# Kernel optimization log

Hardware: AMD Instinct MI355X
Metric: run time of the kernel (lower is better)

The kernel has to match this reference:

```python
import jax, jax.numpy as jnp
import numpy as np

S = 4096          # sequence length (must equal d_model due to the module's v-transpose bug)
D = 4096          # d_model; n_head = heads = 1, bs = 1
SCALE = 64.0      # scale_factor = sqrt(d_model)
W_STD = 0.02      # weight init scale to keep softmax logits sane


def setup_inputs() -> dict:
    k0 = jax.random.key(0)
    ks = jax.random.split(k0, 8)
    return {
        "query": jax.random.normal(ks[0], (1, S, D), jnp.float32),
        "key":   jax.random.normal(ks[1], (1, S, D), jnp.float32),
        "value": jax.random.normal(ks[2], (1, S, D), jnp.float32),
        "Wq": jax.random.normal(ks[3], (D, D), jnp.float32) * W_STD,
        "bq": jnp.zeros((D,), jnp.float32),
        "Wk": jax.random.normal(ks[4], (D, D), jnp.float32) * W_STD,
        "bk": jnp.zeros((D,), jnp.float32),
        "Wv": jax.random.normal(ks[5], (D, D), jnp.float32) * W_STD,
        "bv": jnp.zeros((D,), jnp.float32),
        "Wo": jax.random.normal(ks[6], (D, D), jnp.float32) * W_STD,
        "bo": jnp.zeros((D,), jnp.float32),
    }


def reference(query, key, value, Wq, bq, Wk, bk, Wv, bv, Wo, bo):
    # Linear projections (torch Linear: x @ W.T + b). n_head = 1, so out dim = D.
    q = query @ Wq.T + bq                       # [1, S, D]
    k = key   @ Wk.T + bk                       # [1, S, D]
    v = value @ Wv.T + bv                       # [1, S, D]
    # k.reshape(bs, heads, -1, d_model).transpose(2, 3) -> [1, 1, D, S]
    k4 = k.reshape(1, 1, S, D).transpose(0, 1, 3, 2)
    # v gets the SAME (buggy) transpose -> [1, 1, D, S]
    v4 = v.reshape(1, 1, S, D).transpose(0, 1, 3, 2)
    # q [1,S,D] broadcasts against k4 [1,1,D,S] -> scores [1,1,S,S]
    scores = jnp.matmul(q[:, None], k4) / SCALE
    attn = jax.nn.softmax(scores, axis=-1)      # [1, 1, S, S]
    # dropout_p = 0 / eval mode -> identity
    ctx = jnp.matmul(attn, v4)                  # [1, 1, S, D] (S == D)
    out = ctx @ Wo.T + bo + value[:, None]      # residual add, broadcast to [1,1,S,D]
    return out.reshape(1, -1, D)                # [1, S, D]
```

## Files before the change

kernel.cpp:

```cpp
#include <hip/hip_runtime.h>


typedef __attribute__((ext_vector_type(4))) float f32x4;
typedef __attribute__((ext_vector_type(8))) short short8;
typedef __attribute__((ext_vector_type(4))) unsigned short us4;

#define DIM 4096
#define NT  64

__device__ __forceinline__ unsigned short f2bf(float f) {
    unsigned int u = __builtin_bit_cast(unsigned int, f);
    u += 0x7fffu + ((u >> 16) & 1u);
    return (unsigned short)(u >> 16);
}

__device__ __forceinline__ void gll16(const void* g, void* l) {
    __builtin_amdgcn_global_load_lds(
        (const __attribute__((address_space(1))) unsigned int*)g,
        (__attribute__((address_space(3))) unsigned int*)l,
        16, 0, 0);
}

__global__ void cast_kernel(const float* __restrict__ in, unsigned short* __restrict__ out) {
    const size_t i = ((size_t)blockIdx.x * 256 + threadIdx.x) * 4;
    float4 x = *(const float4*)(in + i);
    us4 y;
    y.x = f2bf(x.x); y.y = f2bf(x.y); y.z = f2bf(x.z); y.w = f2bf(x.w);
    *(us4*)(out + i) = y;
}

template <int EPI>
__global__ __launch_bounds__(512, 2)
void gemm256(const unsigned short* __restrict__ A, const unsigned short* __restrict__ B,
             void* __restrict__ Cout, const float* __restrict__ bias,
             const float* __restrict__ res) {
    __shared__ alignas(16) char lds[131072];

    const int tid = threadIdx.x;
    const int w = tid >> 6, l = tid & 63;
    const int wr = w >> 2, wc = w & 3;

    const int bid = blockIdx.x;
    const int swz = (bid & 7) * 32 + (bid >> 3);
    const int row0 = (swz >> 4) << 8;
    const int col0 = (swz & 15) << 8;

    const int laneA  = (l & 15) * 64 + ((((l >> 4) << 4)) ^ ((l & 8) << 2));
    const int sl_row = l >> 2;
    const int sl_col = ((l & 3) << 3) ^ ((l & 32) ? 16 : 0);

    f32x4 acc[8][4];
    const f32x4 zero = {0.f, 0.f, 0.f, 0.f};
#pragma unroll
    for (int m = 0; m < 8; ++m)
#pragma unroll
        for (int n = 0; n < 4; ++n) acc[m][n] = zero;

    char* const ldsp = (char*)lds;

    auto stage = [&](const unsigned short* __restrict__ M, char* ldsMat, int rowbase,
                     int t, int h) {
        {
            const int rg = h * 8 + (w >> 1), cg = w & 1;
            gll16(M + (size_t)(rowbase + rg * 16 + sl_row) * DIM + t * 64 + cg * 32 + sl_col,
                  ldsMat + ((rg * 2 + cg) << 10));
        }
        {
            const int s = 8 + w;
            const int rg = h * 8 + (s >> 1), cg = s & 1;
            gll16(M + (size_t)(rowbase + rg * 16 + sl_row) * DIM + t * 64 + cg * 32 + sl_col,
                  ldsMat + ((rg * 2 + cg) << 10));
        }
    };

    stage(A, ldsp,          row0, 0, 0);
    stage(A, ldsp,          row0, 0, 1);
    stage(B, ldsp + 32768,  col0, 0, 0);
    stage(B, ldsp + 32768,  col0, 0, 1);
    stage(A, ldsp + 65536,  row0, 1, 0);
    asm volatile("s_waitcnt vmcnt(2)\ns_barrier" ::: "memory");

#pragma unroll 1
    for (int t = 0; t < NT; ++t) {
        const char* Ab = ldsp + (t & 1) * 65536;
        const char* Bb = Ab + 32768;
        const int t1 = (t + 1 < NT) ? t + 1 : NT - 1;
        const int t2 = (t + 2 < NT) ? t + 2 : NT - 1;
        char* A1 = ldsp + (t1 & 1) * 65536;
        char* B1 = A1 + 32768;
        char* A2 = ldsp + (t2 & 1) * 65536;

        const int aoff = wr * 16384 + laneA;
        const int boff = wc * 8192 + laneA;

        short8 a[4][2], b0[2][2], b1[2][2];

#pragma unroll
        for (int m2 = 0; m2 < 4; ++m2)
#pragma unroll
            for (int ks = 0; ks < 2; ++ks)
                a[m2][ks] = *(const short8*)(Ab + aoff + ((m2 * 2 + ks) << 10));
#pragma unroll
        for (int n2 = 0; n2 < 2; ++n2)
#pragma unroll
            for (int ks = 0; ks < 2; ++ks)
                b0[n2][ks] = *(const short8*)(Bb + boff + ((n2 * 2 + ks) << 10));
        stage(A, A1, row0, t1, 1);
        __builtin_amdgcn_s_barrier();
        asm volatile("s_waitcnt lgkmcnt(0)");
        __builtin_amdgcn_s_setprio(1);
#pragma unroll
        for (int m2 = 0; m2 < 4; ++m2)
#pragma unroll
            for (int n2 = 0; n2 < 2; ++n2)
#pragma unroll
                for (int ks = 0; ks < 2; ++ks)
                    acc[m2][n2] = __builtin_amdgcn_mfma_f32_16x16x32_bf16(
                        a[m2][ks], b0[n2][ks], acc[m2][n2], 0, 0, 0);
        __builtin_amdgcn_s_setprio(0);
        __builtin_amdgcn_s_barrier();

#pragma unroll
        for (int n2 = 0; n2 < 2; ++n2)
#pragma unroll
            for (int ks = 0; ks < 2; ++ks)
                b1[n2][ks] = *(const short8*)(Bb + boff + (((2 + n2) * 2 + ks) << 10));
        stage(B, B1, col0, t1, 0);
        __builtin_amdgcn_s_barrier();
        asm volatile("s_waitcnt lgkmcnt(0)");
        __builtin_amdgcn_s_setprio(1);
#pragma unroll
        for (int m2 = 0; m2 < 4; ++m2)
#pragma unroll
            for (int n2 = 0; n2 < 2; ++n2)
#pragma unroll
                for (int ks = 0; ks < 2; ++ks)
                    acc[m2][2 + n2] = __builtin_amdgcn_mfma_f32_16x16x32_bf16(
                        a[m2][ks], b1[n2][ks], acc[m2][2 + n2], 0, 0, 0);
        __builtin_amdgcn_s_setprio(0);
        __builtin_amdgcn_s_barrier();

#pragma unroll
        for (int m2 = 0; m2 < 4; ++m2)
#pragma unroll
            for (int ks = 0; ks < 2; ++ks)
                a[m2][ks] = *(const short8*)(Ab + aoff + (((4 + m2) * 2 + ks) << 10));
        stage(B, B1, col0, t1, 1);
        __builtin_amdgcn_s_barrier();
        asm volatile("s_waitcnt lgkmcnt(0)");
        __builtin_amdgcn_s_setprio(1);
#pragma unroll
        for (int m2 = 0; m2 < 4; ++m2)
#pragma unroll
            for (int n2 = 0; n2 < 2; ++n2)
#pragma unroll
                for (int ks = 0; ks < 2; ++ks)
                    acc[4 + m2][2 + n2] = __builtin_amdgcn_mfma_f32_16x16x32_bf16(
                        a[m2][ks], b1[n2][ks], acc[4 + m2][2 + n2], 0, 0, 0);
        __builtin_amdgcn_s_setprio(0);
        __builtin_amdgcn_s_barrier();

        stage(A, A2, row0, t2, 0);
        __builtin_amdgcn_s_barrier();
        __builtin_amdgcn_s_setprio(1);
#pragma unroll
        for (int m2 = 0; m2 < 4; ++m2)
#pragma unroll
            for (int n2 = 0; n2 < 2; ++n2)
#pragma unroll
                for (int ks = 0; ks < 2; ++ks)
                    acc[4 + m2][n2] = __builtin_amdgcn_mfma_f32_16x16x32_bf16(
                        a[m2][ks], b0[n2][ks], acc[4 + m2][n2], 0, 0, 0);
        __builtin_amdgcn_s_setprio(0);
        asm volatile("s_waitcnt vmcnt(2)\ns_barrier" ::: "memory");
    }
    asm volatile("s_waitcnt vmcnt(0)" ::: "memory");

#pragma unroll
    for (int mf = 0; mf < 8; ++mf) {
        const int grow0 = row0 + wr * 128 + mf * 16 + ((l >> 4) << 2);
#pragma unroll
        for (int nf = 0; nf < 4; ++nf) {
            const int gcol = col0 + wc * 64 + nf * 16 + (l & 15);
            float bias_v = 0.f;
            if constexpr (EPI != 1) {
                if (bias) bias_v = bias[gcol];
            }
#pragma unroll
            for (int r = 0; r < 4; ++r) {
                const size_t idx = (size_t)(grow0 + r) * DIM + gcol;
                const float x = acc[mf][nf][r] + bias_v;
                if constexpr (EPI == 0) {
                    ((unsigned short*)Cout)[idx] = f2bf(x);
                } else if constexpr (EPI == 1) {
                    ((float*)Cout)[idx] = x * 0.015625f;
                } else {
                    ((float*)Cout)[idx] = x + res[idx];
                }
            }
        }
    }
}

__global__ __launch_bounds__(256)
void softmax_kernel(const float* __restrict__ S, unsigned short* __restrict__ P) {
    const int row = blockIdx.x;
    const int t = threadIdx.x;
    const float* src = S + (size_t)row * DIM;

    float v[16];
#pragma unroll
    for (int i = 0; i < 16; ++i) v[i] = src[t + (i << 8)];

    float m = v[0];
#pragma unroll
    for (int i = 1; i < 16; ++i) m = fmaxf(m, v[i]);
#pragma unroll
    for (int off = 32; off > 0; off >>= 1) m = fmaxf(m, __shfl_xor(m, off));

    __shared__ float redm[4], reds[4];
    if ((t & 63) == 0) redm[t >> 6] = m;
    __syncthreads();
    m = fmaxf(fmaxf(redm[0], redm[1]), fmaxf(redm[2], redm[3]));

    float s = 0.f;
#pragma unroll
    for (int i = 0; i < 16; ++i) {
        v[i] = expf(v[i] - m);
        s += v[i];
    }
#pragma unroll
    for (int off = 32; off > 0; off >>= 1) s += __shfl_xor(s, off);
    if ((t & 63) == 0) reds[t >> 6] = s;
    __syncthreads();
    s = (reds[0] + reds[1]) + (reds[2] + reds[3]);

    const float inv = 1.0f / s;
    unsigned short* dst = P + (size_t)row * DIM;
#pragma unroll
    for (int i = 0; i < 16; ++i) dst[t + (i << 8)] = f2bf(v[i] * inv);
}

extern "C" void kernel_launch(void* const* d_in, const int* in_sizes, int n_in,
                              void* d_out, int out_size, void* d_ws, size_t ws_size,
                              hipStream_t stream) {
    const float* query = (const float*)d_in[0];
    const float* key   = (const float*)d_in[1];
    const float* value = (const float*)d_in[2];
    const float* Wq    = (const float*)d_in[3];
    const float* bq    = (const float*)d_in[4];
    const float* Wk    = (const float*)d_in[5];
    const float* bk    = (const float*)d_in[6];
    const float* Wv    = (const float*)d_in[7];
    const float* bv    = (const float*)d_in[8];
    const float* Wo    = (const float*)d_in[9];
    const float* bo    = (const float*)d_in[10];

    const size_t SZ = (size_t)DIM * DIM;
    unsigned short* qb   = (unsigned short*)d_ws;
    unsigned short* kb   = qb + SZ;
    unsigned short* vb   = kb + SZ;
    unsigned short* xb   = vb + SZ;
    unsigned short* wb   = xb + SZ;
    unsigned short* Pb   = wb + SZ;
    unsigned short* ctxb = Pb + SZ;
    float* scores = (float*)(ctxb + SZ);

    const dim3 cg(16384), cb(256);
    const dim3 gg(256), gb(512);

    cast_kernel<<<cg, cb, 0, stream>>>(query, xb);
    cast_kernel<<<cg, cb, 0, stream>>>(Wq, wb);
    gemm256<0><<<gg, gb, 0, stream>>>(xb, wb, qb, bq, nullptr);
    cast_kernel<<<cg, cb, 0, stream>>>(key, xb);
    cast_kernel<<<cg, cb, 0, stream>>>(Wk, wb);
    gemm256<0><<<gg, gb, 0, stream>>>(xb, wb, kb, bk, nullptr);
    cast_kernel<<<cg, cb, 0, stream>>>(value, xb);
    cast_kernel<<<cg, cb, 0, stream>>>(Wv, wb);
    gemm256<0><<<gg, gb, 0, stream>>>(xb, wb, vb, bv, nullptr);
    gemm256<1><<<gg, gb, 0, stream>>>(qb, kb, scores, nullptr, nullptr);
    softmax_kernel<<<4096, 256, 0, stream>>>(scores, Pb);
    gemm256<0><<<gg, gb, 0, stream>>>(Pb, vb, ctxb, nullptr, nullptr);
    cast_kernel<<<cg, cb, 0, stream>>>(Wo, wb);
    gemm256<2><<<gg, gb, 0, stream>>>(ctxb, wb, d_out, bo, value);
}
```

Before: 842.3 us.

## Software-pipeline LDS fragment reads across iterations with register double-buffering

Restructures the GEMM main loop so the first A and B fragments for the next k-tile are read from LDS during the current tile's last MFMA phase, using ping-pong register sets and a 2x unrolled loop body. The explicit lgkmcnt(0) waits are removed and the global-to-LDS staging order is rearranged so the rows needed first land earlier. This is meant to hide LDS read latency behind MFMA work. In exchange it raises register pressure and relies on the compiler to place waits correctly around the reordered barriers.

```diff
diff --git a/kernel.cpp b/kernel.cpp
--- a/kernel.cpp
+++ b/kernel.cpp
@@ -45,7 +45,7 @@
     const int row0 = (swz >> 4) << 8;
     const int col0 = (swz & 15) << 8;
 
-    const int laneA  = (l & 15) * 64 + ((((l >> 4) << 4)) ^ ((l & 8) << 2));
+    const int laneA  = (l & 15) * 64 + (((l >> 4) << 4) ^ ((l & 8) << 2));
     const int sl_row = l >> 2;
     const int sl_col = ((l & 3) << 3) ^ ((l & 32) ? 16 : 0);
 
@@ -57,57 +57,66 @@
         for (int n = 0; n < 4; ++n) acc[m][n] = zero;
 
     char* const ldsp = (char*)lds;
-
-    auto stage = [&](const unsigned short* __restrict__ M, char* ldsMat, int rowbase,
-                     int t, int h) {
-        {
-            const int rg = h * 8 + (w >> 1), cg = w & 1;
-            gll16(M + (size_t)(rowbase + rg * 16 + sl_row) * DIM + t * 64 + cg * 32 + sl_col,
-                  ldsMat + ((rg * 2 + cg) << 10));
-        }
-        {
-            const int s = 8 + w;
-            const int rg = h * 8 + (s >> 1), cg = s & 1;
-            gll16(M + (size_t)(rowbase + rg * 16 + sl_row) * DIM + t * 64 + cg * 32 + sl_col,
-                  ldsMat + ((rg * 2 + cg) << 10));
-        }
+    char* const A0 = ldsp;
+    char* const B0 = ldsp + 32768;
+    char* const A1 = ldsp + 65536;
+    char* const B1 = ldsp + 98304;
+
+    const int aoff = wr * 16384 + laneA;
+    const int boff = wc * 8192 + laneA;
+
+    auto stageA = [&](const unsigned short* __restrict__ M, char* Abase, int base, int t, int h) {
+        const int c1 = w & 1;
+        const int r1 = h * 8 + (w >> 1);
+        gll16(M + (size_t)(base + r1 * 16 + sl_row) * DIM + t * 64 + c1 * 32 + sl_col,
+              Abase + ((r1 * 2 + c1) << 10));
+        const int r2 = h * 8 + 4 + (w >> 1);
+        gll16(M + (size_t)(base + r2 * 16 + sl_row) * DIM + t * 64 + c1 * 32 + sl_col,
+              Abase + ((r2 * 2 + c1) << 10));
     };
-
-    stage(A, ldsp,          row0, 0, 0);
-    stage(A, ldsp,          row0, 0, 1);
-    stage(B, ldsp + 32768,  col0, 0, 0);
-    stage(B, ldsp + 32768,  col0, 0, 1);
-    stage(A, ldsp + 65536,  row0, 1, 0);
+    auto stageB = [&](const unsigned short* __restrict__ M, char* Bbase, int base, int t, int part) {
+        const int c1 = w & 1;
+        const int q1 = w >> 1;
+        const int r1 = ((q1 >> 1) << 2) + (q1 & 1) + part * 2;
+        gll16(M + (size_t)(base + r1 * 16 + sl_row) * DIM + t * 64 + c1 * 32 + sl_col,
+              Bbase + ((r1 * 2 + c1) << 10));
+        const int q2 = 4 + q1;
+        const int r2 = ((q2 >> 1) << 2) + (q2 & 1) + part * 2;
+        gll16(M + (size_t)(base + r2 * 16 + sl_row) * DIM + t * 64 + c1 * 32 + sl_col,
+              Bbase + ((r2 * 2 + c1) << 10));
+    };
+
+    short8 alo[4][2], ahi[4][2], b1r[2][2], b0A[2][2], b0B[2][2];
+
+    stageA(A, A0, row0, 0, 0);
+    stageA(A, A0, row0, 0, 1);
+    stageB(B, B0, col0, 0, 0);
+    stageB(B, B0, col0, 0, 1);
+    stageA(A, A1, row0, 1, 0);
     asm volatile("s_waitcnt vmcnt(2)\ns_barrier" ::: "memory");
-
-#pragma unroll 1
-    for (int t = 0; t < NT; ++t) {
-        const char* Ab = ldsp + (t & 1) * 65536;
-        const char* Bb = Ab + 32768;
+#pragma unroll
+    for (int m2 = 0; m2 < 4; ++m2)
+#pragma unroll
+        for (int ks = 0; ks < 2; ++ks)
+            alo[m2][ks] = *(const short8*)(A0 + aoff + ((m2 * 2 + ks) << 10));
+#pragma unroll
+    for (int n2 = 0; n2 < 2; ++n2)
+#pragma unroll
+        for (int ks = 0; ks < 2; ++ks)
+            b0A[n2][ks] = *(const short8*)(B0 + boff + ((n2 * 2 + ks) << 10));
+
+    auto body = [&](int t, const char* Ab, const char* Bb, char* An, char* Bn, char* Ac,
+                    short8 (&b0c)[2][2], short8 (&b0n)[2][2]) {
         const int t1 = (t + 1 < NT) ? t + 1 : NT - 1;
         const int t2 = (t + 2 < NT) ? t + 2 : NT - 1;
-        char* A1 = ldsp + (t1 & 1) * 65536;
-        char* B1 = A1 + 32768;
-        char* A2 = ldsp + (t2 & 1) * 65536;
-
-        const int aoff = wr * 16384 + laneA;
-        const int boff = wc * 8192 + laneA;
-
-        short8 a[4][2], b0[2][2], b1[2][2];
-
-#pragma unroll
-        for (int m2 = 0; m2 < 4; ++m2)
+
+#pragma unroll
+        for (int n2 = 0; n2 < 2; ++n2)
 #pragma unroll
             for (int ks = 0; ks < 2; ++ks)
-                a[m2][ks] = *(const short8*)(Ab + aoff + ((m2 * 2 + ks) << 10));
-#pragma unroll
-        for (int n2 = 0; n2 < 2; ++n2)
-#pragma unroll
-            for (int ks = 0; ks < 2; ++ks)
-                b0[n2][ks] = *(const short8*)(Bb + boff + ((n2 * 2 + ks) << 10));
-        stage(A, A1, row0, t1, 1);
-        __builtin_amdgcn_s_barrier();
-        asm volatile("s_waitcnt lgkmcnt(0)");
+                b1r[n2][ks] = *(const short8*)(Bb + boff + (((2 + n2) * 2 + ks) << 10));
+        stageA(A, An, row0, t1, 1);
+        __builtin_amdgcn_s_barrier();
         __builtin_amdgcn_s_setprio(1);
 #pragma unroll
         for (int m2 = 0; m2 < 4; ++m2)
@@ -116,18 +125,17 @@
 #pragma unroll
                 for (int ks = 0; ks < 2; ++ks)
                     acc[m2][n2] = __builtin_amdgcn_mfma_f32_16x16x32_bf16(
-                        a[m2][ks], b0[n2][ks], acc[m2][n2], 0, 0, 0);
+                        alo[m2][ks], b0c[n2][ks], acc[m2][n2], 0, 0, 0);
         __builtin_amdgcn_s_setprio(0);
         __builtin_amdgcn_s_barrier();
 
 #pragma unroll
-        for (int n2 = 0; n2 < 2; ++n2)
+        for (int m2 = 0; m2 < 4; ++m2)
 #pragma unroll
             for (int ks = 0; ks < 2; ++ks)
-                b1[n2][ks] = *(const short8*)(Bb + boff + (((2 + n2) * 2 + ks) << 10));
-        stage(B, B1, col0, t1, 0);
-        __builtin_amdgcn_s_barrier();
-        asm volatile("s_waitcnt lgkmcnt(0)");
+                ahi[m2][ks] = *(const short8*)(Ab + aoff + (((4 + m2) * 2 + ks) << 10));
+        stageB(B, Bn, col0, t1, 0);
+        __builtin_amdgcn_s_barrier();
         __builtin_amdgcn_s_setprio(1);
 #pragma unroll
         for (int m2 = 0; m2 < 4; ++m2)
@@ -136,18 +144,12 @@
 #pragma unroll
                 for (int ks = 0; ks < 2; ++ks)
                     acc[m2][2 + n2] = __builtin_amdgcn_mfma_f32_16x16x32_bf16(
-                        a[m2][ks], b1[n2][ks], acc[m2][2 + n2], 0, 0, 0);
+                        alo[m2][ks], b1r[n2][ks], acc[m2][2 + n2], 0, 0, 0);
         __builtin_amdgcn_s_setprio(0);
         __builtin_amdgcn_s_barrier();
 
-#pragma unroll
-        for (int m2 = 0; m2 < 4; ++m2)
-#pragma unroll
-            for (int ks = 0; ks < 2; ++ks)
-                a[m2][ks] = *(const short8*)(Ab + aoff + (((4 + m2) * 2 + ks) << 10));
-        stage(B, B1, col0, t1, 1);
-        __builtin_amdgcn_s_barrier();
-        asm volatile("s_waitcnt lgkmcnt(0)");
+        stageB(B, Bn, col0, t1, 1);
+        __builtin_amdgcn_s_barrier();
         __builtin_amdgcn_s_setprio(1);
 #pragma unroll
         for (int m2 = 0; m2 < 4; ++m2)
@@ -156,11 +158,21 @@
 #pragma unroll
                 for (int ks = 0; ks < 2; ++ks)
                     acc[4 + m2][2 + n2] = __builtin_amdgcn_mfma_f32_16x16x32_bf16(
-                        a[m2][ks], b1[n2][ks], acc[4 + m2][2 + n2], 0, 0, 0);
+                        ahi[m2][ks], b1r[n2][ks], acc[4 + m2][2 + n2], 0, 0, 0);
         __builtin_amdgcn_s_setprio(0);
-        __builtin_amdgcn_s_barrier();
-
-        stage(A, A2, row0, t2, 0);
+        asm volatile("s_waitcnt vmcnt(2)\ns_barrier" ::: "memory");
+
+#pragma unroll
+        for (int m2 = 0; m2 < 4; ++m2)
+#pragma unroll
+            for (int ks = 0; ks < 2; ++ks)
+                alo[m2][ks] = *(const short8*)(An + aoff + ((m2 * 2 + ks) << 10));
+#pragma unroll
+        for (int n2 = 0; n2 < 2; ++n2)
+#pragma unroll
+            for (int ks = 0; ks < 2; ++ks)
+                b0n[n2][ks] = *(const short8*)(Bn + boff + ((n2 * 2 + ks) << 10));
+        stageA(A, Ac, row0, t2, 0);
         __builtin_amdgcn_s_barrier();
         __builtin_amdgcn_s_setprio(1);
 #pragma unroll
@@ -170,9 +182,15 @@
 #pragma unroll
                 for (int ks = 0; ks < 2; ++ks)
                     acc[4 + m2][n2] = __builtin_amdgcn_mfma_f32_16x16x32_bf16(
-                        a[m2][ks], b0[n2][ks], acc[4 + m2][n2], 0, 0, 0);
+                        ahi[m2][ks], b0c[n2][ks], acc[4 + m2][n2], 0, 0, 0);
         __builtin_amdgcn_s_setprio(0);
         asm volatile("s_waitcnt vmcnt(2)\ns_barrier" ::: "memory");
+    };
+
+#pragma unroll 1
+    for (int tt = 0; tt < NT / 2; ++tt) {
+        body(2 * tt,     A0, B0, A1, B1, A0, b0A, b0B);
+        body(2 * tt + 1, A1, B1, A0, B0, A1, b0B, b0A);
     }
     asm volatile("s_waitcnt vmcnt(0)" ::: "memory");
 
```

Measured after the change: 1.288 ms. 1.53x slower.
